# Optimization experiments

Hardware: AMD Instinct MI355X
Metric: run time of the kernel (lower is better)

## Reference

```python
import jax, jax.numpy as jnp
import numpy as np

EPS = 1e-3       # module eps for mask normalization
LN_EPS = 1e-5    # torch LayerNorm default eps


def _layernorm(x, w, b):
    mu = jnp.mean(x, axis=-1, keepdims=True)
    var = jnp.var(x, axis=-1, keepdims=True)
    return (x - mu) * jax.lax.rsqrt(var + LN_EPS) * w + b


def setup_inputs() -> dict:
    key = jax.random.key(0)
    ks = jax.random.split(key, 8)
    N_seq, N_res, c_m, c_h, c_z = 256, 256, 256, 32, 128
    m = jax.random.normal(ks[0], (N_seq, N_res, c_m), jnp.float32)
    mask = jnp.ones((N_seq, N_res), jnp.float32)
    s_m = 1.0 / np.sqrt(c_m)
    ln_w = jnp.ones((c_m,), jnp.float32)
    ln_b = jnp.zeros((c_m,), jnp.float32)
    w1 = jax.random.normal(ks[1], (c_m, c_h), jnp.float32) * s_m
    b1 = jnp.zeros((c_h,), jnp.float32)
    w2 = jax.random.normal(ks[2], (c_m, c_h), jnp.float32) * s_m
    b2 = jnp.zeros((c_h,), jnp.float32)
    # linear_out has init='final' (zeros) in training; use small random so the
    # reference output / gradients are non-trivial for kernel testing.
    w_out = jax.random.normal(ks[3], (c_h * c_h, c_z), jnp.float32) * 0.02
    b_out = jnp.zeros((c_z,), jnp.float32)
    return {"m": m, "mask": mask, "ln_w": ln_w, "ln_b": ln_b,
            "w1": w1, "b1": b1, "w2": w2, "b2": b2,
            "w_out": w_out, "b_out": b_out}


def reference(m, mask, ln_w, ln_b, w1, b1, w2, b2, w_out, b_out):
    # m: [N_seq, N_res, c_m], mask: [N_seq, N_res]
    ln = _layernorm(m, ln_w, ln_b)
    mk = mask[..., None]                                 # [S, N, 1]
    a = (ln @ w1 + b1) * mk                              # [S, N, h]
    b = (ln @ w2 + b2) * mk                              # [S, N, h]
    a = jnp.swapaxes(a, -2, -3)                          # [N, S, h]
    b = jnp.swapaxes(b, -2, -3)                          # [N, S, h]
    # outer product mean over sequences: [N, N, h, h]
    outer = jnp.einsum('isc,jse->ijce', a, b)
    N = outer.shape[0]
    outer = outer.reshape(N, N, -1)                      # [N, N, h*h]
    out = outer @ w_out + b_out                          # [N, N, c_z]
    norm = jnp.einsum('si,sj->ij', mask, mask) + EPS     # [N, N]
    return out / norm[..., None]
```

## Files before the change

kernel.cpp:

```cpp
#include <hip/hip_runtime.h>
#include <hip/hip_bf16.h>
#include <stdint.h>

typedef __bf16 bf16x8 __attribute__((ext_vector_type(8)));
typedef float  f32x4  __attribute__((ext_vector_type(4)));
typedef __attribute__((address_space(1))) uint32_t u32_g;
typedef __attribute__((address_space(3))) uint32_t u32_l;
typedef unsigned short u16;
typedef u16 u16x4 __attribute__((ext_vector_type(4)));

__device__ __forceinline__ void gload16(const void* g, void* l) {
    __builtin_amdgcn_global_load_lds((u32_g*)g, (u32_l*)l, 16, 0, 0);
}

__device__ __forceinline__ u16 bf16bits(float v) {
    __bf16 h = (__bf16)v;
    return __builtin_bit_cast(u16, h);
}

#define WAITV(n) asm volatile("s_waitcnt vmcnt(" #n ")" ::: "memory")
#define BAR() do { __builtin_amdgcn_s_barrier(); \
                   __builtin_amdgcn_sched_barrier(0); } while (0)

__global__ __launch_bounds__(256) void k_prep(const float* __restrict__ w_out,
                                              const float* __restrict__ mask,
                                              const float* __restrict__ w1,
                                              const float* __restrict__ w2,
                                              u16* __restrict__ WT,
                                              u16* __restrict__ WcatT,
                                              float* __restrict__ normv) {
    __shared__ float mcol[256];
    const int b = blockIdx.x, t = threadIdx.x;
    if (b < 512) {
        int idx = b * 256 + t;
        int z = idx >> 10, kc = idx & 1023;
        int c = kc & 31, e = kc >> 5;
        WT[idx] = bf16bits(w_out[(c * 32 + e) * 128 + z]);
    } else if (b < 576) {
        int idx = (b - 512) * 256 + t;
        int n = idx >> 8, k = idx & 255;
        float v = (n < 32) ? w1[k * 32 + n] : w2[k * 32 + (n - 32)];
        WcatT[idx] = bf16bits(v);
    } else {
        int i = b - 576;
        mcol[t] = mask[(size_t)t * 256 + i];
        __syncthreads();
        float acc = 1e-3f;
#pragma unroll 8
        for (int s = 0; s < 256; ++s)
            acc += mcol[s] * mask[(size_t)s * 256 + t];
        normv[i * 256 + t] = acc;
    }
}

__global__ __launch_bounds__(256, 2) void k_lnproj(
        const float* __restrict__ M, const float* __restrict__ mask,
        const float* __restrict__ lnw, const float* __restrict__ lnb,
        const float* __restrict__ b1, const float* __restrict__ b2,
        const u16* __restrict__ WcatT,
        u16* __restrict__ AT, u16* __restrict__ BT) {
    __shared__ __align__(16) u16 sh[32768];
    const int tid = threadIdx.x, lane = tid & 63, w = tid >> 6;
    const int i = blockIdx.x, s0 = blockIdx.y * 64;

#pragma unroll
    for (int p = 0; p < 8; ++p) {
        int flat = p * 256 + tid;
        int r = flat >> 5, slot = flat & 31;
        int gs = slot ^ (r & 7);
        const char* src = (const char*)WcatT + (size_t)r * 512 + (size_t)gs * 16;
        char* dst = (char*)sh + 32768 + (size_t)(p * 256 + (tid & ~63)) * 16;
        gload16(src, dst);
    }

    float4 wv = *(const float4*)(lnw + lane * 4);
    float4 bv = *(const float4*)(lnb + lane * 4);
    float4 xv[16];
#pragma unroll
    for (int it = 0; it < 16; ++it) {
        int s = s0 + w * 16 + it;
        xv[it] = *(const float4*)(M + ((size_t)s * 256 + i) * 256 + lane * 4);
    }
#pragma unroll
    for (int it = 0; it < 16; ++it) {
        int row = w * 16 + it;
        float4 x = xv[it];
        float s1 = x.x + x.y + x.z + x.w;
        float s2 = x.x * x.x + x.y * x.y + x.z * x.z + x.w * x.w;
#pragma unroll
        for (int o = 1; o < 64; o <<= 1) {
            s1 += __shfl_xor(s1, o);
            s2 += __shfl_xor(s2, o);
        }
        float mu   = s1 * 0.00390625f;
        float var  = s2 * 0.00390625f - mu * mu;
        float rstd = rsqrtf(var + 1e-5f);
        u16x4 pk;
        pk[0] = bf16bits((x.x - mu) * rstd * wv.x + bv.x);
        pk[1] = bf16bits((x.y - mu) * rstd * wv.y + bv.y);
        pk[2] = bf16bits((x.z - mu) * rstd * wv.z + bv.z);
        pk[3] = bf16bits((x.w - mu) * rstd * wv.w + bv.w);
        int byte = (row * 512 + lane * 8) ^ ((row & 7) << 4);
        *(u16x4*)((char*)sh + byte) = pk;
    }
    __syncthreads();

    f32x4 acc[4] = {};
#pragma unroll
    for (int kk = 0; kk < 8; ++kk) {
        int kb = kk * 64 + ((lane >> 4) << 4);
        int arow = w * 16 + (lane & 15);
        bf16x8 af = *(const bf16x8*)((const char*)sh +
                     ((arow * 512 + kb) ^ ((arow & 7) << 4)));
#pragma unroll
        for (int f = 0; f < 4; ++f) {
            int nrow = f * 16 + (lane & 15);
            bf16x8 bfr = *(const bf16x8*)((const char*)sh + 32768 +
                          ((nrow * 512 + kb) ^ ((nrow & 7) << 4)));
            acc[f] = __builtin_amdgcn_mfma_f32_16x16x32_bf16(af, bfr, acc[f], 0, 0, 0);
        }
    }

    const int sb = s0 + w * 16 + ((lane >> 4) << 2);
    float mk[4];
#pragma unroll
    for (int r = 0; r < 4; ++r) mk[r] = mask[(size_t)(sb + r) * 256 + i];
#pragma unroll
    for (int f = 0; f < 4; ++f) {
        int col = f * 16 + (lane & 15);
        float bias = (col < 32) ? b1[col] : b2[col - 32];
        u16* dst = ((col < 32) ? AT : BT) + ((size_t)i * 32 + (col & 31)) * 256 + sb;
        u16x4 pk;
#pragma unroll
        for (int r = 0; r < 4; ++r)
            pk[r] = bf16bits((acc[f][r] + bias) * mk[r]);
        *(u16x4*)dst = pk;
    }
}

__global__ __launch_bounds__(512, 4) void k_fused(
        const u16* __restrict__ AT, const u16* __restrict__ BT,
        const u16* __restrict__ WT, const float* __restrict__ normv,
        const float* __restrict__ b_out, float* __restrict__ out) {
    __shared__ __align__(16) u16 sh[36864];
    const int tid  = threadIdx.x;
    const int lane = tid & 63;
    const int wid  = tid >> 6;
    const int wr   = wid >> 2, wc = wid & 3;
    const int l15  = lane & 15;
    const int q16  = lane >> 4;
    const int lid = blockIdx.x;
    const int swz = (lid & 7) * 256 + (lid >> 3);
    const int bx = swz & 63, by = swz >> 6;
    const int m0 = bx * 128, n0 = by * 256;

    f32x4 acc[4][4] = {};

    auto stage = [&](int kt, int buf) {
        char* base = (char*)sh + buf * 24576;
        const int k0 = kt * 32;
        {
            int r = tid >> 2, slot = tid & 3;
            int gs = slot ^ ((r >> 1) & 3);
            gload16((const char*)AT + (((size_t)(m0 + r)) * 256 + k0) * 2 + gs * 16,
                    base + (size_t)(tid & ~63) * 16);
        }
#pragma unroll
        for (int q = 0; q < 2; ++q) {
            int flat = q * 512 + tid;
            int r = flat >> 2, slot = flat & 3;
            int gs = slot ^ ((r >> 1) & 3);
            gload16((const char*)BT + (((size_t)(n0 + r)) * 256 + k0) * 2 + gs * 16,
                    base + 8192 + (size_t)(q * 512 + (tid & ~63)) * 16);
        }
    };

    auto compute = [&](int buf) {
        const char* Ab = (const char*)sh + buf * 24576;
        const char* Bb = Ab + 8192;
        bf16x8 af[4], bfr[4];
#pragma unroll
        for (int mi = 0; mi < 4; ++mi) {
            int rA = wr * 64 + mi * 16 + l15;
            af[mi] = *(const bf16x8*)(Ab + rA * 64 + (q16 ^ ((rA >> 1) & 3)) * 16);
        }
#pragma unroll
        for (int nj = 0; nj < 4; ++nj) {
            int rB = wc * 64 + nj * 16 + l15;
            bfr[nj] = *(const bf16x8*)(Bb + rB * 64 + (q16 ^ ((rB >> 1) & 3)) * 16);
        }
        __builtin_amdgcn_s_setprio(1);
#pragma unroll
        for (int mi = 0; mi < 4; ++mi)
#pragma unroll
            for (int nj = 0; nj < 4; ++nj)
                acc[mi][nj] = __builtin_amdgcn_mfma_f32_16x16x32_bf16(
                    af[mi], bfr[nj], acc[mi][nj], 0, 0, 0);
        __builtin_amdgcn_s_setprio(0);
    };

    stage(0, 0);
    stage(1, 1);
    WAITV(3);
    BAR();
#pragma unroll
    for (int t = 0; t < 8; ++t) {
        if (t + 2 < 8) stage(t + 2, (t + 2) % 3);
        compute(t % 3);
        if (t < 6) { WAITV(3); }
        else if (t == 6) { WAITV(0); }
        BAR();
    }

#pragma unroll
    for (int mi = 0; mi < 4; ++mi)
#pragma unroll
        for (int nj = 0; nj < 4; ++nj) {
            int m = wr * 64 + mi * 16 + (q16 << 2);
            int n = wc * 64 + nj * 16 + l15;
            int pr = ((m >> 5) << 3) | (n >> 5);
            int c0 = m & 31, e = n & 31;
            int byte = pr * 2048 + (e * 32 + c0) * 2;
            byte ^= ((pr ^ e) & 7) << 4;
            u16x4 pk;
#pragma unroll
            for (int r = 0; r < 4; ++r)
                pk[r] = bf16bits(acc[mi][nj][r]);
            *(u16x4*)((char*)sh + byte) = pk;
        }
    __syncthreads();

    f32x4 acc2[2][2] = {};
    const int zb = wid * 16 + l15;
    const int ko = q16 * 8;
    bf16x8 wbr[4];
    bf16x8 par[2][2];
#pragma unroll
    for (int d = 0; d < 3; ++d)
        wbr[d] = *(const bf16x8*)(WT + (size_t)zb * 1024 + d * 32 + ko);
#pragma unroll
    for (int pf = 0; pf < 2; ++pf) {
        int prw = pf * 16 + l15;
        int byte = (prw * 2048 + ko * 2) ^ ((prw & 7) << 4);
        par[0][pf] = *(const bf16x8*)((const char*)sh + byte);
    }
#pragma unroll
    for (int ks = 0; ks < 32; ++ks) {
        if (ks + 3 < 32)
            wbr[(ks + 3) & 3] = *(const bf16x8*)(WT + (size_t)zb * 1024 + (ks + 3) * 32 + ko);
        if (ks + 1 < 32) {
#pragma unroll
            for (int pf = 0; pf < 2; ++pf) {
                int prw = pf * 16 + l15;
                int byte = (prw * 2048 + ((ks + 1) * 32 + ko) * 2)
                           ^ (((prw ^ (ks + 1)) & 7) << 4);
                par[(ks + 1) & 1][pf] = *(const bf16x8*)((const char*)sh + byte);
            }
        }
        __builtin_amdgcn_s_setprio(1);
#pragma unroll
        for (int pf = 0; pf < 2; ++pf)
            acc2[pf][ks & 1] = __builtin_amdgcn_mfma_f32_16x16x32_bf16(
                par[ks & 1][pf], wbr[ks & 3], acc2[pf][ks & 1], 0, 0, 0);
        __builtin_amdgcn_s_setprio(0);
    }

    const int i0 = bx * 4, j0 = by * 8;
#pragma unroll
    for (int pf = 0; pf < 2; ++pf)
#pragma unroll
        for (int r = 0; r < 4; ++r) {
            int pr = pf * 16 + (q16 << 2) + r;
            int z  = zb;
            int i = i0 + (pr >> 3), j = j0 + (pr & 7);
            float val = (acc2[pf][0][r] + acc2[pf][1][r] + b_out[z]) / normv[i * 256 + j];
            out[((size_t)(i * 256 + j)) * 128 + z] = val;
        }
}

extern "C" void kernel_launch(void* const* d_in, const int* in_sizes, int n_in,
                              void* d_out, int out_size, void* d_ws, size_t ws_size,
                              hipStream_t stream) {
    const float* M    = (const float*)d_in[0];
    const float* mask = (const float*)d_in[1];
    const float* lnw  = (const float*)d_in[2];
    const float* lnb  = (const float*)d_in[3];
    const float* w1   = (const float*)d_in[4];
    const float* b1   = (const float*)d_in[5];
    const float* w2   = (const float*)d_in[6];
    const float* b2   = (const float*)d_in[7];
    const float* wout = (const float*)d_in[8];
    const float* bout = (const float*)d_in[9];
    float* out = (float*)d_out;

    char* ws = (char*)d_ws;
    u16*   AT    = (u16*)(ws);
    u16*   BT    = (u16*)(ws + 4194304);
    u16*   WT    = (u16*)(ws + 8388608);
    float* normv = (float*)(ws + 8650752);
    u16*   WcatT = (u16*)(ws + 8912896);

    k_prep  <<<832, 256, 0, stream>>>(wout, mask, w1, w2, WT, WcatT, normv);
    k_lnproj<<<dim3(256, 4), 256, 0, stream>>>(M, mask, lnw, lnb, b1, b2, WcatT, AT, BT);
    k_fused <<<2048, 512, 0, stream>>>(AT, BT, WT, normv, bout, out);
}
```

Baseline: 117.3 us.

## Load B fragments directly to registers and use 32x32 MFMA for projection

The main outer-product GEMM now streams only the A tile through LDS, while B fragments are loaded from global memory straight into registers and prefetched one k-step ahead, interleaved with the MFMAs. This shrinks shared memory and removes the B LDS round trip. The second GEMM (pair-feature times W_out) is switched to 32x32x16 MFMA on only 4 of the 8 waves, each covering 32 output channels with deeper W prefetch. The trade-off is more direct global-load latency exposure and half the waves sitting idle in the epilogue GEMM.

```diff
diff --git a/kernel.cpp b/kernel.cpp
--- a/kernel.cpp
+++ b/kernel.cpp
@@ -4,6 +4,7 @@
 
 typedef __bf16 bf16x8 __attribute__((ext_vector_type(8)));
 typedef float  f32x4  __attribute__((ext_vector_type(4)));
+typedef float  f32x16 __attribute__((ext_vector_type(16)));
 typedef __attribute__((address_space(1))) uint32_t u32_g;
 typedef __attribute__((address_space(3))) uint32_t u32_l;
 typedef unsigned short u16;
@@ -142,7 +143,7 @@
         const u16* __restrict__ AT, const u16* __restrict__ BT,
         const u16* __restrict__ WT, const float* __restrict__ normv,
         const float* __restrict__ b_out, float* __restrict__ out) {
-    __shared__ __align__(16) u16 sh[36864];
+    __shared__ __align__(16) u16 sh[32768];
     const int tid  = threadIdx.x;
     const int lane = tid & 63;
     const int wid  = tid >> 6;
@@ -155,59 +156,47 @@
     const int m0 = bx * 128, n0 = by * 256;
 
     f32x4 acc[4][4] = {};
-
-    auto stage = [&](int kt, int buf) {
-        char* base = (char*)sh + buf * 24576;
-        const int k0 = kt * 32;
-        {
-            int r = tid >> 2, slot = tid & 3;
-            int gs = slot ^ ((r >> 1) & 3);
-            gload16((const char*)AT + (((size_t)(m0 + r)) * 256 + k0) * 2 + gs * 16,
-                    base + (size_t)(tid & ~63) * 16);
-        }
-#pragma unroll
-        for (int q = 0; q < 2; ++q) {
-            int flat = q * 512 + tid;
-            int r = flat >> 2, slot = flat & 3;
-            int gs = slot ^ ((r >> 1) & 3);
-            gload16((const char*)BT + (((size_t)(n0 + r)) * 256 + k0) * 2 + gs * 16,
-                    base + 8192 + (size_t)(q * 512 + (tid & ~63)) * 16);
-        }
+    bf16x8 bfr[4];
+
+    auto stageA = [&](int kt, int buf) {
+        int r = tid >> 2, slot = tid & 3;
+        int gs = slot ^ ((r >> 1) & 3);
+        gload16((const char*)AT + (((size_t)(m0 + r)) * 256 + kt * 32) * 2 + gs * 16,
+                (char*)sh + buf * 8192 + (size_t)(tid & ~63) * 16);
     };
-
-    auto compute = [&](int buf) {
-        const char* Ab = (const char*)sh + buf * 24576;
-        const char* Bb = Ab + 8192;
-        bf16x8 af[4], bfr[4];
+    auto loadB = [&](int nj, int kt) {
+        bfr[nj] = *(const bf16x8*)(BT + ((size_t)(n0 + wc * 64 + nj * 16 + l15)) * 256
+                                      + kt * 32 + q16 * 8);
+    };
+
+    stageA(0, 0);
+#pragma unroll
+    for (int nj = 0; nj < 4; ++nj) loadB(nj, 0);
+    stageA(1, 1);
+    WAITV(1);
+    BAR();
+
+#pragma unroll
+    for (int t = 0; t < 8; ++t) {
+        const char* Ab = (const char*)sh + (t % 3) * 8192;
+        bf16x8 af[4];
 #pragma unroll
         for (int mi = 0; mi < 4; ++mi) {
             int rA = wr * 64 + mi * 16 + l15;
             af[mi] = *(const bf16x8*)(Ab + rA * 64 + (q16 ^ ((rA >> 1) & 3)) * 16);
         }
+        __builtin_amdgcn_s_setprio(1);
 #pragma unroll
         for (int nj = 0; nj < 4; ++nj) {
-            int rB = wc * 64 + nj * 16 + l15;
-            bfr[nj] = *(const bf16x8*)(Bb + rB * 64 + (q16 ^ ((rB >> 1) & 3)) * 16);
-        }
-        __builtin_amdgcn_s_setprio(1);
-#pragma unroll
-        for (int mi = 0; mi < 4; ++mi)
-#pragma unroll
-            for (int nj = 0; nj < 4; ++nj)
+#pragma unroll
+            for (int mi = 0; mi < 4; ++mi)
                 acc[mi][nj] = __builtin_amdgcn_mfma_f32_16x16x32_bf16(
                     af[mi], bfr[nj], acc[mi][nj], 0, 0, 0);
+            if (t + 1 < 8) loadB(nj, t + 1);
+        }
         __builtin_amdgcn_s_setprio(0);
-    };
-
-    stage(0, 0);
-    stage(1, 1);
-    WAITV(3);
-    BAR();
-#pragma unroll
-    for (int t = 0; t < 8; ++t) {
-        if (t + 2 < 8) stage(t + 2, (t + 2) % 3);
-        compute(t % 3);
-        if (t < 6) { WAITV(3); }
+        if (t + 2 < 8) stageA(t + 2, (t + 2) % 3);
+        if (t < 6) { WAITV(1); }
         else if (t == 6) { WAITV(0); }
         BAR();
     }
@@ -230,52 +219,52 @@
         }
     __syncthreads();
 
-    f32x4 acc2[2][2] = {};
-    const int zb = wid * 16 + l15;
-    const int ko = q16 * 8;
-    bf16x8 wbr[4];
-    bf16x8 par[2][2];
-#pragma unroll
-    for (int d = 0; d < 3; ++d)
-        wbr[d] = *(const bf16x8*)(WT + (size_t)zb * 1024 + d * 32 + ko);
-#pragma unroll
-    for (int pf = 0; pf < 2; ++pf) {
-        int prw = pf * 16 + l15;
-        int byte = (prw * 2048 + ko * 2) ^ ((prw & 7) << 4);
-        par[0][pf] = *(const bf16x8*)((const char*)sh + byte);
-    }
-#pragma unroll
-    for (int ks = 0; ks < 32; ++ks) {
-        if (ks + 3 < 32)
-            wbr[(ks + 3) & 3] = *(const bf16x8*)(WT + (size_t)zb * 1024 + (ks + 3) * 32 + ko);
-        if (ks + 1 < 32) {
-#pragma unroll
-            for (int pf = 0; pf < 2; ++pf) {
-                int prw = pf * 16 + l15;
-                int byte = (prw * 2048 + ((ks + 1) * 32 + ko) * 2)
-                           ^ (((prw ^ (ks + 1)) & 7) << 4);
-                par[(ks + 1) & 1][pf] = *(const bf16x8*)((const char*)sh + byte);
+    if (wid < 4) {
+        const int z0  = wid * 32;
+        const int hi  = lane >> 5;
+        const int p32 = lane & 31;
+        const u16* wtrow = WT + (size_t)(z0 + p32) * 1024 + hi * 8;
+
+        f32x16 a0 = {}, a1 = {};
+        bf16x8 wbr[8];
+#pragma unroll
+        for (int d = 0; d < 8; ++d)
+            wbr[d] = *(const bf16x8*)(wtrow + d * 16);
+
+        auto paddr = [&](int ks) {
+            int kc = ks * 16 + hi * 8;
+            int byte = p32 * 2048 + kc * 2;
+            byte ^= ((p32 ^ (kc >> 5)) & 7) << 4;
+            return (const bf16x8*)((const char*)sh + byte);
+        };
+        bf16x8 pa0 = *paddr(0), pa1 = *paddr(1);
+
+#pragma unroll
+        for (int ks = 0; ks < 64; ++ks) {
+            bf16x8 cur = (ks & 1) ? pa1 : pa0;
+            if (ks + 2 < 64) {
+                if (ks & 1) pa1 = *paddr(ks + 2);
+                else        pa0 = *paddr(ks + 2);
             }
-        }
-        __builtin_amdgcn_s_setprio(1);
-#pragma unroll
-        for (int pf = 0; pf < 2; ++pf)
-            acc2[pf][ks & 1] = __builtin_amdgcn_mfma_f32_16x16x32_bf16(
-                par[ks & 1][pf], wbr[ks & 3], acc2[pf][ks & 1], 0, 0, 0);
-        __builtin_amdgcn_s_setprio(0);
-    }
-
-    const int i0 = bx * 4, j0 = by * 8;
-#pragma unroll
-    for (int pf = 0; pf < 2; ++pf)
-#pragma unroll
-        for (int r = 0; r < 4; ++r) {
-            int pr = pf * 16 + (q16 << 2) + r;
-            int z  = zb;
-            int i = i0 + (pr >> 3), j = j0 + (pr & 7);
-            float val = (acc2[pf][0][r] + acc2[pf][1][r] + b_out[z]) / normv[i * 256 + j];
+            if (ks & 1)
+                a1 = __builtin_amdgcn_mfma_f32_32x32x16_bf16(cur, wbr[ks & 7], a1, 0, 0, 0);
+            else
+                a0 = __builtin_amdgcn_mfma_f32_32x32x16_bf16(cur, wbr[ks & 7], a0, 0, 0, 0);
+            if (ks + 8 < 64)
+                wbr[ks & 7] = *(const bf16x8*)(wtrow + (ks + 8) * 16);
+        }
+
+        const int i0 = bx * 4, j0 = by * 8;
+        const int z  = z0 + p32;
+        const float bz = b_out[z];
+#pragma unroll
+        for (int r = 0; r < 16; ++r) {
+            int pair = (r & 3) + 8 * (r >> 2) + 4 * hi;
+            int i = i0 + (pair >> 3), j = j0 + (pair & 7);
+            float val = (a0[r] + a1[r] + bz) / normv[i * 256 + j];
             out[((size_t)(i * 256 + j)) * 128 + z] = val;
         }
+    }
 }
 
 extern "C" void kernel_launch(void* const* d_in, const int* in_sizes, int n_in,
```

Result: slower. 156.5 us (+33.5%).
